# Performance work log

Hardware: AMD Instinct MI355X
Metric: run time of the kernel (lower is better)

## Reference

```python
import jax, jax.numpy as jnp
import numpy as np

D = 256
K = 64


def setup_inputs() -> dict:
    key = jax.random.key(0)
    k1, k2, k3 = jax.random.split(key, 3)
    B, H, W = 16, 96, 96
    X = jax.random.normal(k1, (B, D, H, W), dtype=jnp.float32)
    std1 = 1.0 / float(np.sqrt(K * D))
    std2 = 1.0 / float(np.sqrt(K))
    codewords = jax.random.uniform(k2, (K, D), dtype=jnp.float32, minval=-std1, maxval=std1)
    scale = jax.random.uniform(k3, (K,), dtype=jnp.float32, minval=-std2, maxval=std2)
    return {"X": X, "codewords": codewords, "scale": scale}


def reference(X, codewords, scale):
    # X: [B, D, H, W] -> Xf: [B, N, D]
    B = X.shape[0]
    Xf = X.reshape(B, X.shape[1], -1).transpose(0, 2, 1)
    # Scaled L2 distances: SL[b,n,k] = scale[k] * ||x_bn - c_k||^2
    x2 = jnp.sum(Xf * Xf, axis=-1, keepdims=True)          # [B, N, 1]
    c2 = jnp.sum(codewords * codewords, axis=-1)            # [K]
    xc = jnp.einsum('bnd,kd->bnk', Xf, codewords)           # [B, N, K]
    SL = scale * (x2 - 2.0 * xc + c2)                       # [B, N, K]
    # Assignment weights: softmax over codewords K
    A = jax.nn.softmax(SL, axis=-1)                         # [B, N, K]
    # Aggregate residuals: E[b,k,d] = sum_n A[b,n,k] * (X[b,n,d] - C[k,d])
    E = jnp.einsum('bnk,bnd->bkd', A, Xf) - jnp.sum(A, axis=1)[:, :, None] * codewords
    return E
```

## Files before the change

kernel.cpp:

```cpp
#include <hip/hip_runtime.h>

#define NDIM  256
#define NK    64
#define NPIX  9216
#define NB    16
#define TN    64
#define NW    48
#define TPB   3
#define TILES_PB 144
#define GRID  (NB*NW)

typedef _Float16 half2_t __attribute__((ext_vector_type(2)));
typedef _Float16 half8_t __attribute__((ext_vector_type(8)));
typedef float    f32x4  __attribute__((ext_vector_type(4)));

__device__ __forceinline__ float fdot2(half2_t a, half2_t b, float c) {
  return __builtin_amdgcn_fdot2(a, b, c, false);
}

#define OFF_CH     0
#define OFF_C2     (NK * NDIM / 2)
#define OFF_ASUM   (OFF_C2 + NK)
#define OFF_APART  (OFF_ASUM + NB * NK)
#define OFF_EPART  (OFF_APART + GRID * NK)
#define WS_NEED    ((size_t)OFF_EPART * 4 + (size_t)GRID * NK * NDIM * 2)

__global__ void c2ch_kernel(const float* __restrict__ Cw, float* __restrict__ c2,
                            _Float16* __restrict__ ChH) {
  const int k = blockIdx.x, t = threadIdx.x;
  const float4 v = *(const float4*)(Cw + k * NDIM + 4 * t);
  half2_t h0; h0.x = (_Float16)v.x; h0.y = (_Float16)v.y;
  half2_t h1; h1.x = (_Float16)v.z; h1.y = (_Float16)v.w;
  *(half2_t*)&ChH[k * NDIM + 4 * t]     = h0;
  *(half2_t*)&ChH[k * NDIM + 4 * t + 2] = h1;
  float s = v.x*v.x + v.y*v.y + v.z*v.z + v.w*v.w;
#pragma unroll
  for (int o = 32; o; o >>= 1) s += __shfl_down(s, o);
  if (t == 0) c2[k] = s;
}

__global__ __launch_bounds__(256, 2) void encode_main(
    const float* __restrict__ X, const _Float16* __restrict__ ChH,
    const float* __restrict__ scale, const float* __restrict__ c2,
    void* __restrict__ Eout, float* __restrict__ Aout, int mode)
{
  __shared__ _Float16 XbS[32 * 66 * 8];
  __shared__ _Float16 Al[NK][72];
  __shared__ float red2[4][TN];
  __shared__ float redM[4][TN];
  __shared__ float redS[4][TN];

  const int tid  = threadIdx.x;
  const int w    = __builtin_amdgcn_readfirstlane(tid >> 6);
  const int lane = tid & 63;
  const int m    = lane & 15, quad = lane >> 4;
  const int b    = blockIdx.x / NW;
  const int wid  = blockIdx.x % NW;
  const float* Xbase = X + (size_t)b * NDIM * NPIX;
  const int kbase = w * 16;

  half8_t af1[8];
#pragma unroll
  for (int ks = 0; ks < 8; ++ks)
    af1[ks] = *(const half8_t*)(ChH + (kbase + m) * NDIM + ks * 32 + quad * 8);

  const float4 scv = *(const float4*)(scale + kbase + quad * 4);
  const float4 c2v = *(const float4*)(c2 + kbase + quad * 4);
  const float sc[4] = {scv.x, scv.y, scv.z, scv.w};
  const float sq[4] = {scv.x * c2v.x, scv.y * c2v.y, scv.z * c2v.z, scv.w * c2v.w};

  f32x4 acc_e[4][4];
#pragma unroll
  for (int i = 0; i < 4; ++i)
#pragma unroll
    for (int j = 0; j < 4; ++j)
      acc_e[i][j] = (f32x4){0.f, 0.f, 0.f, 0.f};
  float asum_acc = 0.f;

  for (int tt = 0; tt < TPB; ++tt) {
    const int n0 = (wid + tt * NW) * TN;
    __syncthreads();

    {
      const float* Xg = Xbase + (size_t)(w * 64) * NPIX + n0 + lane;
      float xsq = 0.f;
#pragma unroll
      for (int g = 0; g < 8; ++g) {
        float xv[8];
#pragma unroll
        for (int i = 0; i < 8; ++i) xv[i] = Xg[(size_t)(g * 8 + i) * NPIX];
        half8_t hv;
#pragma unroll
        for (int i = 0; i < 8; ++i) { hv[i] = (_Float16)xv[i]; xsq += xv[i] * xv[i]; }
        *(half8_t*)&XbS[((w * 8 + g) * 66 + lane) * 8] = hv;
      }
      red2[w][lane] = xsq;
    }
    __syncthreads();

    f32x4 accs[4];
#pragma unroll
    for (int nt = 0; nt < 4; ++nt) accs[nt] = (f32x4){0.f, 0.f, 0.f, 0.f};
#pragma unroll
    for (int ks = 0; ks < 8; ++ks) {
#pragma unroll
      for (int nt = 0; nt < 4; ++nt) {
        const half8_t bf = *(const half8_t*)&XbS[((ks * 4 + quad) * 66 + nt * 16 + m) * 8];
        accs[nt] = __builtin_amdgcn_mfma_f32_16x16x32_f16(af1[ks], bf, accs[nt], 0, 0, 0);
      }
    }

    float e[4][4], mw[4];
#pragma unroll
    for (int nt = 0; nt < 4; ++nt) {
      const int p = nt * 16 + m;
      const float x2p = red2[0][p] + red2[1][p] + red2[2][p] + red2[3][p];
      float L[4];
      float mx = -3.0e38f;
#pragma unroll
      for (int r = 0; r < 4; ++r) {
        L[r] = sc[r] * x2p - 2.f * sc[r] * accs[nt][r] + sq[r];
        mx = fmaxf(mx, L[r]);
      }
      mx = fmaxf(mx, __shfl_xor(mx, 16));
      mx = fmaxf(mx, __shfl_xor(mx, 32));
      float s = 0.f;
#pragma unroll
      for (int r = 0; r < 4; ++r) { e[nt][r] = __expf(L[r] - mx); s += e[nt][r]; }
      s += __shfl_xor(s, 16);
      s += __shfl_xor(s, 32);
      mw[nt] = mx;
      if (lane < 16) { redM[w][p] = mx; redS[w][p] = s; }
    }
    __syncthreads();
#pragma unroll
    for (int nt = 0; nt < 4; ++nt) {
      const int p = nt * 16 + m;
      const float M = fmaxf(fmaxf(redM[0][p], redM[1][p]),
                            fmaxf(redM[2][p], redM[3][p]));
      const float T = redS[0][p] * __expf(redM[0][p] - M)
                    + redS[1][p] * __expf(redM[1][p] - M)
                    + redS[2][p] * __expf(redM[2][p] - M)
                    + redS[3][p] * __expf(redM[3][p] - M);
      const float norm = __expf(mw[nt] - M) / T;
#pragma unroll
      for (int r = 0; r < 4; ++r)
        Al[kbase + quad * 4 + r][p] = (_Float16)(e[nt][r] * norm);
    }
    __syncthreads();

#pragma unroll
    for (int ks = 0; ks < 2; ++ks) {
      half8_t ba[4];
#pragma unroll
      for (int kt = 0; kt < 4; ++kt)
        ba[kt] = *(const half8_t*)&Al[kt * 16 + m][ks * 32 + quad * 8];
#pragma unroll
      for (int dt = 0; dt < 4; ++dt) {
        const int c = w * 8 + dt * 2 + (m >> 3);
        const int dlow = m & 7;
        half8_t xa;
#pragma unroll
        for (int j = 0; j < 8; ++j)
          xa[j] = XbS[(c * 66 + ks * 32 + quad * 8 + j) * 8 + dlow];
#pragma unroll
        for (int kt = 0; kt < 4; ++kt)
          acc_e[dt][kt] = __builtin_amdgcn_mfma_f32_16x16x32_f16(xa, ba[kt], acc_e[dt][kt], 0, 0, 0);
      }
    }
    if (tid < NK) {
      const half2_t one = {(_Float16)1.f, (_Float16)1.f};
#pragma unroll
      for (int lc = 0; lc < 8; ++lc) {
        const half8_t sv = *(const half8_t*)&Al[tid][lc * 8];
        asum_acc = fdot2(__builtin_shufflevector(sv, sv, 0, 1), one, asum_acc);
        asum_acc = fdot2(__builtin_shufflevector(sv, sv, 2, 3), one, asum_acc);
        asum_acc = fdot2(__builtin_shufflevector(sv, sv, 4, 5), one, asum_acc);
        asum_acc = fdot2(__builtin_shufflevector(sv, sv, 6, 7), one, asum_acc);
      }
    }
  }

  __syncthreads();
  _Float16* Et = XbS;
#pragma unroll
  for (int dt = 0; dt < 4; ++dt)
#pragma unroll
    for (int kt = 0; kt < 4; ++kt)
#pragma unroll
      for (int r = 0; r < 4; ++r) {
        const int k = kt * 16 + m;
        const int d = w * 64 + dt * 16 + quad * 4 + r;
        Et[k * 264 + d] = (_Float16)acc_e[dt][kt][r];
      }
  __syncthreads();
  const int ko = tid >> 2, cq = tid & 3;
  if (mode) {
    _Float16* Ebk = (_Float16*)Eout + (size_t)blockIdx.x * (NK * NDIM);
#pragma unroll
    for (int g = 0; g < 8; ++g)
      *(half8_t*)&Ebk[ko * NDIM + cq * 64 + g * 8] =
          *(const half8_t*)&Et[ko * 264 + cq * 64 + g * 8];
    if (tid < NK) Aout[blockIdx.x * NK + tid] = asum_acc;
  } else {
    float* Ebk = (float*)Eout + (size_t)b * (NK * NDIM);
#pragma unroll
    for (int g = 0; g < 64; ++g)
      atomicAdd(&Ebk[ko * NDIM + cq * 64 + g], (float)Et[ko * 264 + cq * 64 + g]);
    if (tid < NK) atomicAdd(&Aout[b * NK + tid], asum_acc);
  }
}

__global__ void asum_reduce_kernel(const float* __restrict__ Apart,
                                   float* __restrict__ asum) {
  const int i = blockIdx.x * 256 + threadIdx.x;
  const int bb = i >> 6, k = i & 63;
  float s = 0.f;
  for (int w = 0; w < NW; ++w) s += Apart[(bb * NW + w) * NK + k];
  asum[i] = s;
}

__global__ void finalize_partials(const _Float16* __restrict__ EpartH,
                                  const float* __restrict__ asum,
                                  const float* __restrict__ Cw,
                                  float* __restrict__ out) {
  const int i = blockIdx.x * 256 + threadIdx.x;
  const int bb = i >> 14;
  const int o  = i & 16383;
  const int k  = o >> 8, d = i & 255;
  float s = 0.f;
#pragma unroll 4
  for (int w = 0; w < NW; ++w)
    s += (float)EpartH[((size_t)(bb * NW + w) << 14) + o];
  out[i] = s - asum[bb * NK + k] * Cw[k * NDIM + d];
}

__global__ void finalize_atomic(const float* __restrict__ E_acc,
                                const float* __restrict__ asum,
                                const float* __restrict__ Cw,
                                float* __restrict__ out) {
  const int i = blockIdx.x * 256 + threadIdx.x;
  const int d = i & 255;
  const int k = (i >> 8) & 63;
  const int bb = i >> 14;
  out[i] = E_acc[i] - asum[bb * NK + k] * Cw[k * NDIM + d];
}

extern "C" void kernel_launch(void* const* d_in, const int* in_sizes, int n_in,
                              void* d_out, int out_size, void* d_ws, size_t ws_size,
                              hipStream_t stream) {
  const float* X     = (const float*)d_in[0];
  const float* Cw    = (const float*)d_in[1];
  const float* scale = (const float*)d_in[2];
  float* out = (float*)d_out;

  float* wsf = (float*)d_ws;
  _Float16* ChH = (_Float16*)(wsf + OFF_CH);
  float* c2     = wsf + OFF_C2;
  float* asum   = wsf + OFF_ASUM;
  float* Apart  = wsf + OFF_APART;

  c2ch_kernel<<<NK, 64, 0, stream>>>(Cw, c2, ChH);
  if (ws_size >= WS_NEED) {
    _Float16* EpartH = (_Float16*)(wsf + OFF_EPART);
    encode_main<<<GRID, 256, 0, stream>>>(X, ChH, scale, c2, EpartH, Apart, 1);
    asum_reduce_kernel<<<4, 256, 0, stream>>>(Apart, asum);
    finalize_partials<<<(NB*NK*NDIM)/256, 256, 0, stream>>>(EpartH, asum, Cw, out);
  } else {
    float* E_acc = wsf + OFF_APART;
    hipMemsetAsync(wsf + OFF_ASUM, 0,
                   (size_t)(NB*NK + GRID*NK + NB*NK*NDIM) * sizeof(float), stream);
    encode_main<<<GRID, 256, 0, stream>>>(X, ChH, scale, c2, E_acc, asum, 0);
    finalize_atomic<<<(NB*NK*NDIM)/256, 256, 0, stream>>>(E_acc, asum, Cw, out);
  }
}
```

Baseline: 253.6 us.

## Prefetch next X tile into registers and vectorize finalize reduction

The main kernel now loads the next pixel tile of X into a 64-float register array right after the current tile is staged to shared memory, so global loads overlap with the MFMA and softmax work. The partial-sum finalize kernel now has each thread handle 8 outputs, using half8 vector loads and float4 stores, and the asum reduction loop is unrolled. The register prefetch adds 64 VGPRs per thread, which may lower occupancy or cause spills.

```diff
diff --git a/kernel.cpp b/kernel.cpp
--- a/kernel.cpp
+++ b/kernel.cpp
@@ -7,7 +7,6 @@
 #define TN    64
 #define NW    48
 #define TPB   3
-#define TILES_PB 144
 #define GRID  (NB*NW)
 
 typedef _Float16 half2_t __attribute__((ext_vector_type(2)));
@@ -77,26 +76,37 @@
       acc_e[i][j] = (f32x4){0.f, 0.f, 0.f, 0.f};
   float asum_acc = 0.f;
 
+  float xv[64];
+  {
+    const float* Xg = Xbase + (size_t)(w * 64) * NPIX + wid * TN + lane;
+#pragma unroll
+    for (int i = 0; i < 64; ++i) xv[i] = Xg[(size_t)i * NPIX];
+  }
+
   for (int tt = 0; tt < TPB; ++tt) {
-    const int n0 = (wid + tt * NW) * TN;
     __syncthreads();
 
     {
-      const float* Xg = Xbase + (size_t)(w * 64) * NPIX + n0 + lane;
       float xsq = 0.f;
 #pragma unroll
       for (int g = 0; g < 8; ++g) {
-        float xv[8];
-#pragma unroll
-        for (int i = 0; i < 8; ++i) xv[i] = Xg[(size_t)(g * 8 + i) * NPIX];
         half8_t hv;
 #pragma unroll
-        for (int i = 0; i < 8; ++i) { hv[i] = (_Float16)xv[i]; xsq += xv[i] * xv[i]; }
+        for (int i = 0; i < 8; ++i) {
+          const float v = xv[g * 8 + i];
+          hv[i] = (_Float16)v; xsq += v * v;
+        }
         *(half8_t*)&XbS[((w * 8 + g) * 66 + lane) * 8] = hv;
       }
       red2[w][lane] = xsq;
     }
     __syncthreads();
+
+    if (tt + 1 < TPB) {
+      const float* Xg = Xbase + (size_t)(w * 64) * NPIX + (wid + (tt + 1) * NW) * TN + lane;
+#pragma unroll
+      for (int i = 0; i < 64; ++i) xv[i] = Xg[(size_t)i * NPIX];
+    }
 
     f32x4 accs[4];
 #pragma unroll
@@ -216,6 +226,7 @@
   const int i = blockIdx.x * 256 + threadIdx.x;
   const int bb = i >> 6, k = i & 63;
   float s = 0.f;
+#pragma unroll 8
   for (int w = 0; w < NW; ++w) s += Apart[(bb * NW + w) * NK + k];
   asum[i] = s;
 }
@@ -224,15 +235,31 @@
                                   const float* __restrict__ asum,
                                   const float* __restrict__ Cw,
                                   float* __restrict__ out) {
-  const int i = blockIdx.x * 256 + threadIdx.x;
-  const int bb = i >> 14;
-  const int o  = i & 16383;
-  const int k  = o >> 8, d = i & 255;
-  float s = 0.f;
+  const int g = blockIdx.x * 256 + threadIdx.x;
+  const int i0 = g * 8;
+  const int bb = i0 >> 14;
+  const int o  = i0 & 16383;
+  const int k  = o >> 8, d = i0 & 255;
+  float s[8];
+#pragma unroll
+  for (int j = 0; j < 8; ++j) s[j] = 0.f;
+  const _Float16* base = EpartH + (((size_t)bb * NW) << 14) + o;
 #pragma unroll 4
-  for (int w = 0; w < NW; ++w)
-    s += (float)EpartH[((size_t)(bb * NW + w) << 14) + o];
-  out[i] = s - asum[bb * NK + k] * Cw[k * NDIM + d];
+  for (int w = 0; w < NW; ++w) {
+    const half8_t v = *(const half8_t*)(base + ((size_t)w << 14));
+#pragma unroll
+    for (int j = 0; j < 8; ++j) s[j] += (float)v[j];
+  }
+  const float a = asum[bb * NK + k];
+  const float4 c0 = *(const float4*)(Cw + k * NDIM + d);
+  const float4 c1 = *(const float4*)(Cw + k * NDIM + d + 4);
+  float4 r0, r1;
+  r0.x = s[0] - a * c0.x; r0.y = s[1] - a * c0.y;
+  r0.z = s[2] - a * c0.z; r0.w = s[3] - a * c0.w;
+  r1.x = s[4] - a * c1.x; r1.y = s[5] - a * c1.y;
+  r1.z = s[6] - a * c1.z; r1.w = s[7] - a * c1.w;
+  *(float4*)(out + i0)     = r0;
+  *(float4*)(out + i0 + 4) = r1;
 }
 
 __global__ void finalize_atomic(const float* __restrict__ E_acc,
@@ -265,7 +292,7 @@
     _Float16* EpartH = (_Float16*)(wsf + OFF_EPART);
     encode_main<<<GRID, 256, 0, stream>>>(X, ChH, scale, c2, EpartH, Apart, 1);
     asum_reduce_kernel<<<4, 256, 0, stream>>>(Apart, asum);
-    finalize_partials<<<(NB*NK*NDIM)/256, 256, 0, stream>>>(EpartH, asum, Cw, out);
+    finalize_partials<<<(NB*NK*NDIM)/(256*8), 256, 0, stream>>>(EpartH, asum, Cw, out);
   } else {
     float* E_acc = wsf + OFF_APART;
     hipMemsetAsync(wsf + OFF_ASUM, 0,
```

After: 243.0 us. 1.04x faster.
